# Kernel optimization log

Hardware: AMD Instinct MI355X
Metric: run time of the kernel (lower is better)

Reference implementation:

```python
import jax, jax.numpy as jnp
import numpy as np

T, B, V, S = 800, 32, 1024, 100
BLANK = 0
LS = 0.1
NEG = -1e10  # finite 'log-zero' to keep grads NaN-free


def setup_inputs() -> dict:
    key = jax.random.key(0)
    k1, k2, k3, k4 = jax.random.split(key, 4)
    logits = jax.random.normal(k1, (T, B, V), jnp.float32)
    log_probs = jax.nn.log_softmax(logits, axis=-1)  # (T,B,V) as F.ctc_loss expects
    targets = jax.random.randint(k2, (B, S), 1, V)   # non-blank labels
    input_lengths = jax.random.randint(k3, (B,), T // 2, T + 1)
    target_lengths = jax.random.randint(k4, (B,), S // 2, S + 1)
    return dict(log_probs=log_probs, targets=targets,
                input_lengths=input_lengths, target_lengths=target_lengths)


def _ctc_loss_mean(log_probs, targets, input_lengths, target_lengths):
    # log_probs: (T,B,V); targets: (B,S)
    Tt, Bb, Vv = log_probs.shape
    Ss = targets.shape[1]
    L = 2 * Ss + 1  # extended label sequence: blank-interleaved
    ext = jnp.full((Bb, L), BLANK, dtype=targets.dtype).at[:, 1::2].set(targets)
    ext_prev2 = jnp.pad(ext[:, :-2], ((0, 0), (2, 0)), constant_values=BLANK)
    # transition s-2 -> s allowed only for non-blank labels differing from two back
    can_skip = (ext != BLANK) & (ext != ext_prev2)  # (B,L)

    def emit(lp_t):  # (B,V) -> (B,L) emission log-probs of extended labels
        return jnp.take_along_axis(lp_t, ext, axis=1)

    e0 = emit(log_probs[0])
    alpha0 = jnp.full((Bb, L), NEG, dtype=log_probs.dtype)
    alpha0 = alpha0.at[:, 0].set(e0[:, 0]).at[:, 1].set(e0[:, 1])

    def step(alpha, xs):
        lp_t, t = xs
        a1 = jnp.pad(alpha[:, :-1], ((0, 0), (1, 0)), constant_values=NEG)
        a2 = jnp.pad(alpha[:, :-2], ((0, 0), (2, 0)), constant_values=NEG)
        new = jnp.logaddexp(alpha, a1)
        new = jnp.where(can_skip, jnp.logaddexp(new, a2), new) + emit(lp_t)
        # freeze alpha for t >= input_length so final carry == alpha at len-1
        alpha = jnp.where((t < input_lengths)[:, None], new, alpha)
        return alpha, None

    alpha_T, _ = jax.lax.scan(step, alpha0, (log_probs[1:], jnp.arange(1, Tt)))

    idx = 2 * target_lengths  # final blank position in extended sequence
    a_blank = jnp.take_along_axis(alpha_T, idx[:, None], axis=1)[:, 0]
    a_label = jnp.take_along_axis(alpha_T, (idx - 1)[:, None], axis=1)[:, 0]
    nll = -jnp.logaddexp(a_blank, a_label)  # (B,)
    nll = jnp.where(nll > 1e9, 0.0, nll)    # zero_infinity
    # reduction='mean': per-sample loss / target_length, then batch mean
    return jnp.mean(nll / target_lengths.astype(log_probs.dtype))


def reference(log_probs, targets, input_lengths, target_lengths):
    ctc = _ctc_loss_mean(log_probs, targets, input_lengths, target_lengths)
    smooth = -jnp.mean(log_probs)
    return (1.0 - LS) * ctc + LS * smooth
```

## Files before the change

kernel.cpp:

```cpp
#include <hip/hip_runtime.h>
#include <hip/hip_bf16.h>

#define T_DIM 800
#define B_DIM 32
#define V_DIM 1024
#define S_DIM 100
#define L2E  1.4426950408889634f
#define LN2  0.6931471805599453f

#define NB1  1600
#define EOFF 4096
#define EROW 128
#define BROWS 801


__device__ __forceinline__ float dpp_shr1_f(float x) {
    return __int_as_float(__builtin_amdgcn_update_dpp(
        0, __float_as_int(x), 0x138, 0xF, 0xF, false));
}
__device__ __forceinline__ int dpp_shr1_i(int x) {
    return __builtin_amdgcn_update_dpp(0, x, 0x138, 0xF, 0xF, false);
}
__device__ __forceinline__ float rl50(float x) {
    return __int_as_float(__builtin_amdgcn_readlane(__float_as_int(x), 50));
}
__device__ __forceinline__ void gl16(const float* g, float* lds_dst) {
    __builtin_amdgcn_global_load_lds(
        (const __attribute__((address_space(1))) unsigned int*)g,
        (__attribute__((address_space(3))) unsigned int*)lds_dst,
        16, 0, 0);
}

extern "C" __global__ void __launch_bounds__(256)
ctc_prep(const float* __restrict__ lp,
         const int* __restrict__ tgt,
         float* __restrict__ ws)
{
    __shared__ float rb[4][2][V_DIM];
    __shared__ float red[4];
    float* E = ws + EOFF;
    float* partials = ws + 1;
    const int bid = blockIdx.x;
    const int tid = threadIdx.x;
    const int w = tid >> 6, j = tid & 63;
    const int b  = bid / 50;
    const int t0 = (bid - b * 50) * 16 + w * 4;
    const int* tg = tgt + b * S_DIM;

    if (bid == 0 && tid == 0) ((unsigned int*)ws)[0] = 0;

    int c1 = 0, c2 = 0;
    if (j <= 49) { int2 t2 = ((const int2*)tg)[j]; c1 = t2.x; c2 = t2.y; }

    float s = 0.0f;
    #pragma unroll
    for (int i = 0; i < 4; ++i) {
        const int t = t0 + i;
        const float4* src = (const float4*)(lp + ((size_t)t * B_DIM + b) * V_DIM);
        float4 va = src[j], vb = src[j + 64], vc = src[j + 128], vd = src[j + 192];
        s += ((va.x + va.y) + (va.z + va.w)) + ((vb.x + vb.y) + (vb.z + vb.w))
           + ((vc.x + vc.y) + (vc.z + vc.w)) + ((vd.x + vd.y) + (vd.z + vd.w));
        float* rw = rb[w][i & 1];
        ((float4*)rw)[j] = va; ((float4*)rw)[j + 64] = vb;
        ((float4*)rw)[j + 128] = vc; ((float4*)rw)[j + 192] = vd;
        float a, c;
        if (j <= 49)      { a = __builtin_amdgcn_exp2f(rw[c1] * L2E);
                            c = __builtin_amdgcn_exp2f(rw[c2] * L2E); }
        else if (j == 50) { float ebv = __builtin_amdgcn_exp2f(rw[0] * L2E);
                            a = ebv; c = ebv; }
        else              { a = 0.0f; c = 0.0f; }
        ((float2*)(E + ((size_t)b * BROWS + t) * EROW))[j] = make_float2(a, c);
    }
    for (int off = 32; off; off >>= 1) s += __shfl_down(s, off, 64);
    if (j == 0) red[w] = s;
    __syncthreads();
    if (tid == 0) partials[bid] = (red[0] + red[1]) + (red[2] + red[3]);
}

extern "C" __global__ void __launch_bounds__(64)
ctc_rec(const int* __restrict__ tgt,
        const int* __restrict__ ilen,
        const int* __restrict__ tlen,
        float* __restrict__ ws,
        float* __restrict__ out)
{
    __shared__ float bufA[32 * EROW];
    __shared__ float bufB[32 * EROW];
    unsigned int* cnt = (unsigned int*)ws;
    float* partials = ws + 1;
    float* nlls = ws + 1 + NB1;
    const int b = blockIdx.x;
    const int l = threadIdx.x;
    const float* E = ws + EOFF + (size_t)b * BROWS * EROW;
    const int* tg = tgt + b * S_DIM;
    const int len = ilen[b];
    const int tl  = tlen[b];
    const int steps = len - 1;

    float cs1f = 0, cs3f = 0;
    if (l <= 49) {
        int v1 = tg[2 * l];
        int vp = (l >= 1) ? tg[2 * l - 1] : -1;
        cs1f = (v1 != vp) ? 1.0f : 0.0f;
        int v3 = tg[2 * l + 1];
        cs3f = (v3 != v1) ? 1.0f : 0.0f;
    }

    float p0 = 0, p1 = 0, p2 = 0, p3 = 0;
    float qv = 0, sff = 0, sfg = 0;
    int   el = 0, eLp = 0;
    {
        float2 q0 = ((const float2*)E)[l];
        float eb0 = rl50(q0.x);
        p0 = (l == 0) ? eb0  : 0.0f;
        p1 = (l == 0) ? q0.x : 0.0f;
    }

    float2 ga0, ga1, ga2, ga3, gb0, gb1, gb2, gb3;

#define STAGE(BUF, SB) do { \
    const int tb_ = 1 + 32 * (SB); \
    _Pragma("unroll") \
    for (int g_ = 0; g_ < 16; ++g_) { \
        gl16(E + (size_t)(tb_ + 2 * g_) * EROW + 4 * l, &BUF[g_ * 256]); \
    } \
} while (0)

#define WAIT0 do { \
    asm volatile("s_waitcnt vmcnt(0)" ::: "memory"); \
    __builtin_amdgcn_sched_barrier(0); \
} while (0)

#define PREF_(BUF, G, R0, R1, R2, R3) do { \
    const float2* bp_ = (const float2*)(BUF); \
    R0 = bp_[(4 * (G) + 0) * 64 + l]; \
    R1 = bp_[(4 * (G) + 1) * 64 + l]; \
    R2 = bp_[(4 * (G) + 2) * 64 + l]; \
    R3 = bp_[(4 * (G) + 3) * 64 + l]; \
} while (0)

#define BD do { \
    float mz_ = fmaxf(fmaxf(p0, p1), fmaxf(p2, p3)); \
    int dead_ = (mz_ == 0.0f) ? 1 : 0; \
    int er_ = (int)((__float_as_uint(mz_) >> 23) & 255u); \
    unsigned fld_ = dead_ ? 127u : (unsigned)(254 - er_); \
    float sc_ = __uint_as_float(fld_ << 23); \
    p0 *= sc_; p1 *= sc_; p2 *= sc_; p3 *= sc_; \
    el += dead_ ? 0 : (er_ - 127); \
    int e1s_ = dpp_shr1_i(el); \
    int elA_ = dead_ ? e1s_ : el; \
    int e2s_ = dpp_shr1_i(elA_); \
    int elB_ = dead_ ? e2s_ : el; \
    int e3s_ = dpp_shr1_i(elB_); \
    int d1_ = e3s_ - elB_; d1_ = d1_ < -120 ? -120 : (d1_ > 120 ? 120 : d1_); \
    int d2_ = eLp  - elB_; d2_ = d2_ < -120 ? -120 : (d2_ > 120 ? 120 : d2_); \
    sfg = (l == 0) ? 0.0f : __uint_as_float((unsigned)(d1_ + 127) << 23); \
    sff = (l == 0) ? 0.0f : __uint_as_float((unsigned)(d2_ + 127) << 23); \
    el = elB_; eLp = e3s_; \
} while (0)

#define ST(SF, Q, EBS) do { \
    float h3_ = qv * (SF); \
    float vown_ = fmaf(cs3f, p1, p2 + p3); \
    float n3_ = vown_ * (Q).y; \
    float n0_ = (p0 + h3_) * (EBS); \
    float n1_ = fmaf(cs1f, h3_, p0 + p1) * (Q).x; \
    float n2_ = (p1 + p2) * (EBS); \
    qv = dpp_shr1_f(n3_); \
    p0 = n0_; p1 = n1_; p2 = n2_; p3 = n3_; \
} while (0)

#define GRP_(R0, R1, R2, R3) do { \
    BD; \
    ST(sff, R0, rl50(R0.x)); \
    ST(sfg, R1, rl50(R1.x)); \
    ST(sfg, R2, rl50(R2.x)); \
    ST(sfg, R3, rl50(R3.x)); \
} while (0)

#define GRPT_(R0, R1, R2, R3, BASE) do { \
    if ((BASE) < nst) { \
        BD; \
        ST(sff, R0, rl50(R0.x)); \
        if ((BASE) + 1 < nst) ST(sfg, R1, rl50(R1.x)); \
        if ((BASE) + 2 < nst) ST(sfg, R2, rl50(R2.x)); \
        if ((BASE) + 3 < nst) ST(sfg, R3, rl50(R3.x)); \
    } \
} while (0)

#define CONS_FULL(BUF) do { \
    PREF_(BUF, 0, ga0, ga1, ga2, ga3); \
    PREF_(BUF, 1, gb0, gb1, gb2, gb3); GRP_(ga0, ga1, ga2, ga3); \
    PREF_(BUF, 2, ga0, ga1, ga2, ga3); GRP_(gb0, gb1, gb2, gb3); \
    PREF_(BUF, 3, gb0, gb1, gb2, gb3); GRP_(ga0, ga1, ga2, ga3); \
    PREF_(BUF, 4, ga0, ga1, ga2, ga3); GRP_(gb0, gb1, gb2, gb3); \
    PREF_(BUF, 5, gb0, gb1, gb2, gb3); GRP_(ga0, ga1, ga2, ga3); \
    PREF_(BUF, 6, ga0, ga1, ga2, ga3); GRP_(gb0, gb1, gb2, gb3); \
    PREF_(BUF, 7, gb0, gb1, gb2, gb3); GRP_(ga0, ga1, ga2, ga3); \
    GRP_(gb0, gb1, gb2, gb3); \
} while (0)

#define CONS_TAIL(BUF) do { \
    PREF_(BUF, 0, ga0, ga1, ga2, ga3); \
    PREF_(BUF, 1, gb0, gb1, gb2, gb3); GRPT_(ga0, ga1, ga2, ga3, 0); \
    PREF_(BUF, 2, ga0, ga1, ga2, ga3); GRPT_(gb0, gb1, gb2, gb3, 4); \
    PREF_(BUF, 3, gb0, gb1, gb2, gb3); GRPT_(ga0, ga1, ga2, ga3, 8); \
    PREF_(BUF, 4, ga0, ga1, ga2, ga3); GRPT_(gb0, gb1, gb2, gb3, 12); \
    PREF_(BUF, 5, gb0, gb1, gb2, gb3); GRPT_(ga0, ga1, ga2, ga3, 16); \
    PREF_(BUF, 6, ga0, ga1, ga2, ga3); GRPT_(gb0, gb1, gb2, gb3, 20); \
    PREF_(BUF, 7, gb0, gb1, gb2, gb3); GRPT_(ga0, ga1, ga2, ga3, 24); \
    GRPT_(gb0, gb1, gb2, gb3, 28); \
} while (0)

    const int nfull = steps >> 5;
    const int nst   = steps & 31;

    STAGE(bufA, 0);
    WAIT0;
    int sb = 0;
    #pragma unroll 1
    for (; sb + 2 <= nfull; sb += 2) {
        STAGE(bufB, sb + 1);
        CONS_FULL(bufA);
        WAIT0;
        STAGE(bufA, sb + 2);
        CONS_FULL(bufB);
        WAIT0;
    }
    if (sb < nfull) {
        STAGE(bufB, sb + 1);
        CONS_FULL(bufA);
        WAIT0;
        CONS_TAIL(bufB);
    } else {
        CONS_TAIL(bufA);
    }

    int idx = 2 * tl;
    int lanehi = idx >> 2, rhi = idx & 3;
    int lanelo = (idx - 1) >> 2, rlo = (idx - 1) & 3;
    float q0 = __shfl(p0, lanehi, 64), q1 = __shfl(p1, lanehi, 64);
    float q2 = __shfl(p2, lanehi, 64), q3 = __shfl(p3, lanehi, 64);
    int   eh = __shfl(el, lanehi, 64);
    float ph = (rhi == 0) ? q0 : (rhi == 1) ? q1 : (rhi == 2) ? q2 : q3;
    float g0 = __shfl(p0, lanelo, 64), g1 = __shfl(p1, lanelo, 64);
    float g2 = __shfl(p2, lanelo, 64), g3 = __shfl(p3, lanelo, 64);
    int   eo = __shfl(el, lanelo, 64);
    float pl = (rlo == 0) ? g0 : (rlo == 1) ? g1 : (rlo == 2) ? g2 : g3;
    float vhi = (ph > 0.0f) ? __builtin_amdgcn_logf(ph) + (float)eh : -3.0e9f;
    float vlo = (pl > 0.0f) ? __builtin_amdgcn_logf(pl) + (float)eo : -3.0e9f;
    float m = fmaxf(vhi, vlo);
    float d = fminf(vhi, vlo) - m;
    float ll2 = m + __builtin_amdgcn_logf(1.0f + __builtin_amdgcn_exp2f(d));
    float nll = -ll2 * LN2;
    if (!(nll < 1e9f)) nll = 0.0f;

    int last = 0;
    if (l == 0) {
        nlls[b] = nll;
        __threadfence();
        unsigned old = __hip_atomic_fetch_add(cnt, 1u, __ATOMIC_ACQ_REL,
                                              __HIP_MEMORY_SCOPE_AGENT);
        last = (old == B_DIM - 1) ? 1 : 0;
    }
    last = __shfl(last, 0, 64);
    if (last) {
        float ps = 0.0f;
        for (int i = l; i < NB1; i += 64) ps += partials[i];
        for (int off = 32; off; off >>= 1) ps += __shfl_down(ps, off, 64);
        float cs = 0.0f;
        if (l < B_DIM) cs = nlls[l] / (float)tlen[l];
        for (int off = 32; off; off >>= 1) cs += __shfl_down(cs, off, 64);
        if (l == 0) {
            float smooth = -ps / (float)((long long)T_DIM * B_DIM * V_DIM);
            float ctc = cs / (float)B_DIM;
            out[0] = 0.9f * ctc + 0.1f * smooth;
        }
    }
}

extern "C" void kernel_launch(void* const* d_in, const int* in_sizes, int n_in,
                              void* d_out, int out_size, void* d_ws, size_t ws_size,
                              hipStream_t stream) {
    const float* lp  = (const float*)d_in[0];
    const int* tgt   = (const int*)d_in[1];
    const int* ilen  = (const int*)d_in[2];
    const int* tlen  = (const int*)d_in[3];
    float* out = (float*)d_out;
    float* ws  = (float*)d_ws;
    ctc_prep<<<NB1, 256, 0, stream>>>(lp, tgt, ws);
    ctc_rec<<<B_DIM, 64, 0, stream>>>(tgt, ilen, tlen, ws, out);
}
```

Baseline: 72.20 us.

## Split ctc_rec into producer wave for LDS staging and consumer compute wave

```diff
diff --git a/kernel.cpp b/kernel.cpp
--- a/kernel.cpp
+++ b/kernel.cpp
@@ -77,7 +77,7 @@
     if (tid == 0) partials[bid] = (red[0] + red[1]) + (red[2] + red[3]);
 }
 
-extern "C" __global__ void __launch_bounds__(64)
+extern "C" __global__ void __launch_bounds__(128)
 ctc_rec(const int* __restrict__ tgt,
         const int* __restrict__ ilen,
         const int* __restrict__ tlen,
@@ -90,12 +90,42 @@
     float* partials = ws + 1;
     float* nlls = ws + 1 + NB1;
     const int b = blockIdx.x;
-    const int l = threadIdx.x;
+    const int tid = threadIdx.x;
+    const int wav = tid >> 6;
+    const int l = tid & 63;
     const float* E = ws + EOFF + (size_t)b * BROWS * EROW;
     const int* tg = tgt + b * S_DIM;
     const int len = ilen[b];
     const int tl  = tlen[b];
     const int steps = len - 1;
+    const int nfull = steps >> 5;
+    const int nst   = steps & 31;
+    const int N     = nfull + (nst ? 1 : 0);
+
+#define STAGE_P(BUFP, SB) do { \
+    const int tb_ = 1 + 32 * (SB); \
+    float* bp_ = (BUFP); \
+    _Pragma("unroll") \
+    for (int g_ = 0; g_ < 16; ++g_) { \
+        gl16(E + (size_t)(tb_ + 2 * g_) * EROW + 4 * l, bp_ + g_ * 256); \
+    } \
+} while (0)
+
+#define WAIT0 do { \
+    asm volatile("s_waitcnt vmcnt(0)" ::: "memory"); \
+    __builtin_amdgcn_sched_barrier(0); \
+} while (0)
+
+    if (wav == 1) {
+        STAGE_P(bufA, 0); WAIT0;
+        __builtin_amdgcn_s_barrier();
+        #pragma unroll 1
+        for (int k = 1; k < N; ++k) {
+            STAGE_P((k & 1) ? bufB : bufA, k); WAIT0;
+            __builtin_amdgcn_s_barrier();
+        }
+        return;
+    }
 
     float cs1f = 0, cs3f = 0;
     if (l <= 49) {
@@ -117,19 +147,6 @@
     }
 
     float2 ga0, ga1, ga2, ga3, gb0, gb1, gb2, gb3;
-
-#define STAGE(BUF, SB) do { \
-    const int tb_ = 1 + 32 * (SB); \
-    _Pragma("unroll") \
-    for (int g_ = 0; g_ < 16; ++g_) { \
-        gl16(E + (size_t)(tb_ + 2 * g_) * EROW + 4 * l, &BUF[g_ * 256]); \
-    } \
-} while (0)
-
-#define WAIT0 do { \
-    asm volatile("s_waitcnt vmcnt(0)" ::: "memory"); \
-    __builtin_amdgcn_sched_barrier(0); \
-} while (0)
 
 #define PREF_(BUF, G, R0, R1, R2, R3) do { \
     const float2* bp_ = (const float2*)(BUF); \
@@ -212,28 +229,16 @@
     GRPT_(gb0, gb1, gb2, gb3, 28); \
 } while (0)
 
-    const int nfull = steps >> 5;
-    const int nst   = steps & 31;
-
-    STAGE(bufA, 0);
-    WAIT0;
-    int sb = 0;
+    __builtin_amdgcn_s_barrier();
     #pragma unroll 1
-    for (; sb + 2 <= nfull; sb += 2) {
-        STAGE(bufB, sb + 1);
-        CONS_FULL(bufA);
-        WAIT0;
-        STAGE(bufA, sb + 2);
-        CONS_FULL(bufB);
-        WAIT0;
-    }
-    if (sb < nfull) {
-        STAGE(bufB, sb + 1);
-        CONS_FULL(bufA);
-        WAIT0;
-        CONS_TAIL(bufB);
-    } else {
-        CONS_TAIL(bufA);
+    for (int k = 0; k + 1 < N; ++k) {
+        const float* cur = (k & 1) ? bufB : bufA;
+        CONS_FULL(cur);
+        __builtin_amdgcn_s_barrier();
+    }
+    {
+        const float* cur = ((N - 1) & 1) ? bufB : bufA;
+        if (nst) { CONS_TAIL(cur); } else { CONS_FULL(cur); }
     }
 
     int idx = 2 * tl;
@@ -289,5 +294,5 @@
     float* out = (float*)d_out;
     float* ws  = (float*)d_ws;
     ctc_prep<<<NB1, 256, 0, stream>>>(lp, tgt, ws);
-    ctc_rec<<<B_DIM, 64, 0, stream>>>(tgt, ilen, tlen, ws, out);
-}
+    ctc_rec<<<B_DIM, 128, 0, stream>>>(tgt, ilen, tlen, ws, out);
+}
```

After: 64.59 us (median of 2 runs). 10.5% less time.
